# Performance work log

Measured on AMD Instinct MI355X. Metric: run time of the kernel, lower is better.

Reference implementation:

```python
import jax, jax.numpy as jnp
import numpy as np

B, N, K = 256, 1024, 64          # batch, atoms per structure, abc combinations
E = 2 * K                        # embedding_dim = 128
NSG = 230                        # number of space groups
LN_EPS = 1e-5


def setup_inputs() -> dict:
    key = jax.random.key(0)
    ks = jax.random.split(key, 12)
    xav = float(np.sqrt(6.0 / (K + K)))  # xavier_uniform bound for [K,K] slices
    return {
        "atom_positions": jax.random.uniform(ks[0], (B, N, 3), dtype=jnp.float32),
        "reciprocal_matrices": jax.random.normal(ks[1], (B, 3, 3), dtype=jnp.float32),
        "space_group": jax.random.randint(ks[2], (B, 1), 1, NSG + 1, dtype=jnp.int32),
        "abc_combinations": jax.random.normal(ks[3], (K, 3), dtype=jnp.float32),
        "graphs_array": jax.random.uniform(ks[4], (NSG, K, K), dtype=jnp.float32),
        "w_real": jax.random.uniform(ks[5], (NSG, K, K), jnp.float32, -xav, xav),
        "w_imag": jax.random.uniform(ks[6], (NSG, K, K), jnp.float32, -xav, xav),
        "b_real": jnp.zeros((NSG, K), jnp.float32),
        "b_imag": jnp.zeros((NSG, K), jnp.float32),
        "W2": jax.random.normal(ks[7], (E, E), dtype=jnp.float32) * 0.05,
        "b2": jnp.zeros((E,), jnp.float32),
        "gamma": jnp.ones((E,), jnp.float32),
        "beta": jnp.zeros((E,), jnp.float32),
    }


def reference(atom_positions, reciprocal_matrices, space_group, abc_combinations,
              graphs_array, w_real, w_imag, b_real, b_imag, W2, b2, gamma, beta):
    sg = space_group[:, 0] - 1                                  # [B] in [0,229]
    # transformed_abc = abc @ recip^T : [B,K,3]
    t_abc = jnp.einsum('kc,bdc->bkd', abc_combinations, reciprocal_matrices)
    # encodings = exp(i*2pi * pos @ t_abc^T) : [B,N,K] complex
    phase = (2.0 * jnp.pi) * jnp.einsum('bnc,bkc->bnk', atom_positions, t_abc)
    enc = jax.lax.complex(jnp.cos(phase), jnp.sin(phase))
    # per-sample adjacency gather + complex batched matmul
    adj = graphs_array[sg]                                      # [B,K,K]
    weighted = jnp.einsum('bnk,bkm->bnm', enc, adj.astype(enc.dtype))
    weighted = weighted[:, :, :K]                               # slice to embedding_dim//2
    # SpaceGroupDenseLayer: per-sample complex expert weights
    Wc = jax.lax.complex(w_real, w_imag)[sg]                    # [B,K,K]
    bc = jax.lax.complex(b_real, b_imag)[sg][:, None, :]        # [B,1,K]
    out_c = jnp.einsum('bni,bif->bnf', weighted, Wc) + bc       # [B,N,K] complex
    x = jnp.concatenate([out_c.real, out_c.imag], axis=-1)      # [B,N,2K]
    x = jax.nn.silu(x)
    x = x @ W2.T + b2                                           # Linear(E,E)
    mu = jnp.mean(x, axis=-1, keepdims=True)
    var = jnp.mean(jnp.square(x - mu), axis=-1, keepdims=True)
    return (x - mu) * jax.lax.rsqrt(var + LN_EPS) * gamma + beta
```

## Files before the change

kernel.cpp:

```cpp
#include <hip/hip_runtime.h>
#include <math.h>

#define BB 256
#define NN 1024
#define KK 64
#define EE 128
#define TM 64

typedef _Float16 half8 __attribute__((ext_vector_type(8)));
typedef __fp16 fp16x2 __attribute__((ext_vector_type(2)));
typedef float f32x4 __attribute__((ext_vector_type(4)));

__device__ __forceinline__ int swz(int row, int halfcol) {
    return (row * EE + halfcol) ^ ((row & 7) << 3);
}
__device__ __forceinline__ int swz64(int row, int halfcol) {
    return (row << 6) + (halfcol ^ ((row & 7) << 3));
}

__device__ __forceinline__ void gload_lds16(const void* g, void* l) {
    __builtin_amdgcn_global_load_lds(
        (const __attribute__((address_space(1))) unsigned int*)g,
        (__attribute__((address_space(3))) unsigned int*)l, 16, 0, 0);
}

__global__ __launch_bounds__(256) void prep_kernel(
    const float* __restrict__ recip,
    const int* __restrict__ space_group,
    const float* __restrict__ abc,
    const float* __restrict__ graphs,
    const float* __restrict__ w_real,
    const float* __restrict__ w_imag,
    const float* __restrict__ b_real,
    const float* __restrict__ b_imag,
    const float* __restrict__ W2,
    _Float16* __restrict__ Mt,
    float* __restrict__ bbout,
    float* __restrict__ tabcP,
    _Float16* __restrict__ W2h)
{
    const int b = blockIdx.x;
    const int t = threadIdx.x;
    const int sg = space_group[b] - 1;

    if (b < EE * EE / 256) {
        const int idx = b * 256 + t;
        W2h[idx] = (_Float16)W2[idx];
    }

    __shared__ float adjL[KK * KK];
    __shared__ float wrL[KK * KK];
    __shared__ float wiL[KK * KK];

    const float* adjG = graphs + (size_t)sg * KK * KK;
    const float* wrG  = w_real + (size_t)sg * KK * KK;
    const float* wiG  = w_imag + (size_t)sg * KK * KK;
    for (int idx = t; idx < KK * KK; idx += 256) {
        adjL[idx] = adjG[idx];
        wrL[idx]  = wrG[idx];
        wiL[idx]  = wiG[idx];
    }
    __syncthreads();

    const int i  = t >> 2;
    const int f0 = (t & 3) * 16;
    float cr[16], ci[16];
#pragma unroll
    for (int c = 0; c < 16; ++c) { cr[c] = 0.f; ci[c] = 0.f; }
    for (int k = 0; k < KK; ++k) {
        const float a = adjL[i * KK + k];
#pragma unroll
        for (int c = 0; c < 16; ++c) {
            cr[c] += a * wrL[k * KK + f0 + c];
            ci[c] += a * wiL[k * KK + f0 + c];
        }
    }
    _Float16* Mb = Mt + (size_t)b * EE * EE;
#pragma unroll
    for (int c = 0; c < 16; ++c) {
        const int f = f0 + c;
        Mb[f * EE + i]             = (_Float16)cr[c];
        Mb[f * EE + KK + i]        = (_Float16)(-ci[c]);
        Mb[(KK + f) * EE + i]      = (_Float16)ci[c];
        Mb[(KK + f) * EE + KK + i] = (_Float16)cr[c];
    }
    if (t < EE) {
        bbout[b * EE + t] = (t < KK) ? b_real[sg * KK + t] : b_imag[sg * KK + (t - KK)];
    }
    if (t < KK) {
        const float a0 = abc[t * 3 + 0], a1 = abc[t * 3 + 1], a2 = abc[t * 3 + 2];
        const float* R = recip + b * 9;
        float4 v;
        v.x = a0 * R[0] + a1 * R[1] + a2 * R[2];
        v.y = a0 * R[3] + a1 * R[4] + a2 * R[5];
        v.z = a0 * R[6] + a1 * R[7] + a2 * R[8];
        v.w = 0.f;
        *(float4*)&tabcP[((size_t)b * KK + t) * 4] = v;
    }
}

__global__ __launch_bounds__(256, 4) void main_kernel(
    const float* __restrict__ pos,
    const _Float16* __restrict__ Mt,
    const float* __restrict__ bball,
    const float* __restrict__ tabcP,
    const _Float16* __restrict__ W2h,
    const float* __restrict__ b2,
    const float* __restrict__ gamma,
    const float* __restrict__ beta,
    float* __restrict__ out)
{
    const int d = blockIdx.x;
    const int j  = d >> 3;
    const int b  = (d & 7) * 32 + (j >> 4);
    const int n0 = (j & 15) * TM;
    const int t  = threadIdx.x;
    const int w    = t >> 6;
    const int lane = t & 63;
    const int ln15 = lane & 15;
    const int kg   = lane >> 4;

    __shared__ __align__(16) _Float16 Bt[EE * EE];
    _Float16* X = Bt + (EE * EE) / 2;

    {
        const char* srcM = (const char*)(Mt + (size_t)b * EE * EE);
#pragma unroll
        for (int i = 0; i < 8; ++i) {
            const int c16 = t + i * 256;
            const int row = c16 >> 4;
            const int sl  = c16 & 15;
            const int g   = row * 16 + (sl ^ (row & 7));
            gload_lds16(srcM + g * 16, (char*)Bt + c16 * 16);
        }
    }

    const int grow = n0 + w * 16 + ln15;
    const float* pr = pos + ((size_t)b * NN + grow) * 3;
    const float px = pr[0], py = pr[1], pz = pr[2];
    const float* tp = tabcP + (size_t)b * KK * 4;

    half8 afrag[4];
#pragma unroll
    for (int mq = 0; mq < 2; ++mq) {
        _Float16 cb[8], sb[8];
#pragma unroll
        for (int jj = 0; jj < 8; ++jj) {
            const int k = mq * 32 + kg * 8 + jj;
            const float4 tv = *(const float4*)&tp[k * 4];
            const float rev = px * tv.x + py * tv.y + pz * tv.z;
            const float fr  = __builtin_amdgcn_fractf(rev);
            sb[jj] = (_Float16)__builtin_amdgcn_sinf(fr);
            cb[jj] = (_Float16)__builtin_amdgcn_cosf(fr);
        }
        afrag[mq]     = *(half8*)cb;
        afrag[mq + 2] = *(half8*)sb;
    }
    __syncthreads();

    __builtin_amdgcn_s_setprio(1);
    f32x4 acc[8];
#pragma unroll
    for (int nt = 0; nt < 8; ++nt) {
        const int n = nt * 16 + ln15;
        f32x4 a = {0.f, 0.f, 0.f, 0.f};
#pragma unroll
        for (int kc = 0; kc < 4; ++kc) {
            const half8 bf = *(const half8*)&Bt[swz(n, kc * 32 + kg * 8)];
            a = __builtin_amdgcn_mfma_f32_16x16x32_f16(bf, afrag[kc], a, 0, 0, 0);
        }
        acc[nt] = a;
    }
    __builtin_amdgcn_s_setprio(0);
    __syncthreads();

    {
        const char* srcW = (const char*)W2h;
#pragma unroll
        for (int i = 0; i < 4; ++i) {
            const int c = t + i * 256;
            const int n = c >> 3;
            const int s = c & 7;
            const int g = n * 16 + (s ^ (n & 7));
            gload_lds16(srcW + g * 16, (char*)Bt + c * 16);
        }
    }

    {
        const int xrow = w * 16 + ln15;
        const float* bbp = bball + b * EE;
#pragma unroll
        for (int nt = 0; nt < 8; ++nt) {
            const int cb0 = nt * 16 + kg * 4;
            const float4 bb4 = *(const float4*)&bbp[cb0];
            float sv[4];
            sv[0] = acc[nt][0] + bb4.x;
            sv[1] = acc[nt][1] + bb4.y;
            sv[2] = acc[nt][2] + bb4.z;
            sv[3] = acc[nt][3] + bb4.w;
#pragma unroll
            for (int r2 = 0; r2 < 4; ++r2)
                sv[r2] = sv[r2] * __builtin_amdgcn_rcpf(1.f + __expf(-sv[r2]));
            const fp16x2 p0 = __builtin_amdgcn_cvt_pkrtz(sv[0], sv[1]);
            const fp16x2 p1 = __builtin_amdgcn_cvt_pkrtz(sv[2], sv[3]);
            uint2 u;
            u.x = __builtin_bit_cast(unsigned int, p0);
            u.y = __builtin_bit_cast(unsigned int, p1);
            *(uint2*)&X[swz(xrow, cb0)] = u;
        }
    }

    const int arow = w * 16 + ln15;
    half8 a2[4];
#pragma unroll
    for (int kc = 0; kc < 4; ++kc)
        a2[kc] = *(const half8*)&X[swz(arow, kc * 32 + kg * 8)];
    __syncthreads();

    {
        const char* srcW = (const char*)W2h;
#pragma unroll
        for (int i = 0; i < 4; ++i) {
            const int c = t + i * 256;
            const int n = c >> 3;
            const int s = c & 7;
            const int g = n * 16 + 8 + (s ^ (n & 7));
            gload_lds16(srcW + g * 16, (char*)X + c * 16);
        }
    }

    __builtin_amdgcn_s_setprio(1);
    f32x4 acc2[8];
#pragma unroll
    for (int nt = 0; nt < 8; ++nt) {
        const int n = nt * 16 + ln15;
        f32x4 a = {0.f, 0.f, 0.f, 0.f};
#pragma unroll
        for (int kc = 0; kc < 2; ++kc) {
            const half8 bf = *(const half8*)&Bt[swz64(n, kc * 32 + kg * 8)];
            a = __builtin_amdgcn_mfma_f32_16x16x32_f16(a2[kc], bf, a, 0, 0, 0);
        }
        acc2[nt] = a;
    }
    __builtin_amdgcn_s_setprio(0);
    __syncthreads();

    __builtin_amdgcn_s_setprio(1);
#pragma unroll
    for (int nt = 0; nt < 8; ++nt) {
        const int n = nt * 16 + ln15;
        f32x4 a = acc2[nt];
#pragma unroll
        for (int kc = 0; kc < 2; ++kc) {
            const half8 bf = *(const half8*)&X[swz64(n, kc * 32 + kg * 8)];
            a = __builtin_amdgcn_mfma_f32_16x16x32_f16(a2[2 + kc], bf, a, 0, 0, 0);
        }
        acc2[nt] = a;
    }
    __builtin_amdgcn_s_setprio(0);

    float s[4] = {0.f, 0.f, 0.f, 0.f}, q[4] = {0.f, 0.f, 0.f, 0.f};
#pragma unroll
    for (int nt = 0; nt < 8; ++nt) {
        const int col = nt * 16 + ln15;
        const float b2v = b2[col];
#pragma unroll
        for (int r2 = 0; r2 < 4; ++r2) {
            const float v = acc2[nt][r2] + b2v;
            acc2[nt][r2] = v;
            s[r2] += v;
            q[r2] += v * v;
        }
    }
#pragma unroll
    for (int m = 1; m < 16; m <<= 1) {
#pragma unroll
        for (int r2 = 0; r2 < 4; ++r2) {
            s[r2] += __shfl_xor(s[r2], m);
            q[r2] += __shfl_xor(q[r2], m);
        }
    }
    const float inv = 1.f / EE;
    float mu[4], rs[4];
#pragma unroll
    for (int r2 = 0; r2 < 4; ++r2) {
        mu[r2] = s[r2] * inv;
        rs[r2] = __builtin_amdgcn_rsqf(fmaxf(q[r2] * inv - mu[r2] * mu[r2], 0.f) + 1e-5f);
    }
#pragma unroll
    for (int nt = 0; nt < 8; ++nt) {
        const int col = nt * 16 + ln15;
        const float g  = gamma[col];
        const float be = beta[col];
#pragma unroll
        for (int r2 = 0; r2 < 4; ++r2) {
            const int rr = w * 16 + kg * 4 + r2;
            out[((size_t)b * NN + n0 + rr) * EE + col] =
                (acc2[nt][r2] - mu[r2]) * rs[r2] * g + be;
        }
    }
}

extern "C" void kernel_launch(void* const* d_in, const int* in_sizes, int n_in,
                              void* d_out, int out_size, void* d_ws, size_t ws_size,
                              hipStream_t stream) {
    const float* pos    = (const float*)d_in[0];
    const float* recip  = (const float*)d_in[1];
    const int*   sgp    = (const int*)d_in[2];
    const float* abc    = (const float*)d_in[3];
    const float* graphs = (const float*)d_in[4];
    const float* wr     = (const float*)d_in[5];
    const float* wi     = (const float*)d_in[6];
    const float* br     = (const float*)d_in[7];
    const float* bi     = (const float*)d_in[8];
    const float* W2     = (const float*)d_in[9];
    const float* b2     = (const float*)d_in[10];
    const float* gm     = (const float*)d_in[11];
    const float* bt     = (const float*)d_in[12];
    float* out = (float*)d_out;

    char* ws = (char*)d_ws;
    _Float16* Mt    = (_Float16*)ws;
    char* p = ws + (size_t)BB * EE * EE * 2;
    _Float16* W2h   = (_Float16*)p;            p += EE * EE * 2;
    float*    bball = (float*)p;               p += (size_t)BB * EE * 4;
    float*    tabcP = (float*)p;

    hipLaunchKernelGGL(prep_kernel, dim3(BB), dim3(256), 0, stream,
                       recip, sgp, abc, graphs, wr, wi, br, bi, W2, Mt, bball, tabcP, W2h);
    hipLaunchKernelGGL(main_kernel, dim3(BB * NN / TM), dim3(256), 0, stream,
                       pos, Mt, bball, tabcP, W2h, b2, gm, bt, out);
}
```

Baseline: 62.98 us.

## Process two 64-row tiles per block to reuse staged matrices

Each block now handles 128 atom rows as two 64-row sub-tiles, so the per-sample fused matrix and the W2 halves loaded into shared memory are reused across twice the rows and the grid halves. The aim is to cut global-to-LDS staging traffic and per-block setup and barrier overhead. In exchange each thread holds twice the accumulators (acc0/acc1, acc2_0/acc2_1, a2_0/a2_1), which raises register pressure and may reduce occupancy under the launch bounds of 4 blocks per CU.

```diff
diff --git a/kernel.cpp b/kernel.cpp
--- a/kernel.cpp
+++ b/kernel.cpp
@@ -112,8 +112,8 @@
 {
     const int d = blockIdx.x;
     const int j  = d >> 3;
-    const int b  = (d & 7) * 32 + (j >> 4);
-    const int n0 = (j & 15) * TM;
+    const int b  = (d & 7) * 32 + (j >> 3);
+    const int n0 = (j & 7) * (2 * TM);
     const int t  = threadIdx.x;
     const int w    = t >> 6;
     const int lane = t & 63;
@@ -135,31 +135,32 @@
         }
     }
 
-    const int grow = n0 + w * 16 + ln15;
-    const float* pr = pos + ((size_t)b * NN + grow) * 3;
-    const float px = pr[0], py = pr[1], pz = pr[2];
     const float* tp = tabcP + (size_t)b * KK * 4;
+    const int rbase = n0 + w * 16 + ln15;
 
     half8 afrag[4];
-#pragma unroll
-    for (int mq = 0; mq < 2; ++mq) {
-        _Float16 cb[8], sb[8];
-#pragma unroll
-        for (int jj = 0; jj < 8; ++jj) {
-            const int k = mq * 32 + kg * 8 + jj;
-            const float4 tv = *(const float4*)&tp[k * 4];
-            const float rev = px * tv.x + py * tv.y + pz * tv.z;
-            const float fr  = __builtin_amdgcn_fractf(rev);
-            sb[jj] = (_Float16)__builtin_amdgcn_sinf(fr);
-            cb[jj] = (_Float16)__builtin_amdgcn_cosf(fr);
-        }
-        afrag[mq]     = *(half8*)cb;
-        afrag[mq + 2] = *(half8*)sb;
+    {
+        const float* pr = pos + ((size_t)b * NN + rbase) * 3;
+        const float px = pr[0], py = pr[1], pz = pr[2];
+#pragma unroll
+        for (int mq = 0; mq < 2; ++mq) {
+            _Float16 cb[8], sb[8];
+#pragma unroll
+            for (int jj = 0; jj < 8; ++jj) {
+                const int k = mq * 32 + kg * 8 + jj;
+                const float4 tv = *(const float4*)&tp[k * 4];
+                const float fr = __builtin_amdgcn_fractf(px * tv.x + py * tv.y + pz * tv.z);
+                sb[jj] = (_Float16)__builtin_amdgcn_sinf(fr);
+                cb[jj] = (_Float16)__builtin_amdgcn_cosf(fr);
+            }
+            afrag[mq]     = *(half8*)cb;
+            afrag[mq + 2] = *(half8*)sb;
+        }
     }
     __syncthreads();
 
     __builtin_amdgcn_s_setprio(1);
-    f32x4 acc[8];
+    f32x4 acc0[8];
 #pragma unroll
     for (int nt = 0; nt < 8; ++nt) {
         const int n = nt * 16 + ln15;
@@ -169,7 +170,41 @@
             const half8 bf = *(const half8*)&Bt[swz(n, kc * 32 + kg * 8)];
             a = __builtin_amdgcn_mfma_f32_16x16x32_f16(bf, afrag[kc], a, 0, 0, 0);
         }
-        acc[nt] = a;
+        acc0[nt] = a;
+    }
+    __builtin_amdgcn_s_setprio(0);
+
+    {
+        const float* pr = pos + ((size_t)b * NN + rbase + TM) * 3;
+        const float px = pr[0], py = pr[1], pz = pr[2];
+#pragma unroll
+        for (int mq = 0; mq < 2; ++mq) {
+            _Float16 cb[8], sb[8];
+#pragma unroll
+            for (int jj = 0; jj < 8; ++jj) {
+                const int k = mq * 32 + kg * 8 + jj;
+                const float4 tv = *(const float4*)&tp[k * 4];
+                const float fr = __builtin_amdgcn_fractf(px * tv.x + py * tv.y + pz * tv.z);
+                sb[jj] = (_Float16)__builtin_amdgcn_sinf(fr);
+                cb[jj] = (_Float16)__builtin_amdgcn_cosf(fr);
+            }
+            afrag[mq]     = *(half8*)cb;
+            afrag[mq + 2] = *(half8*)sb;
+        }
+    }
+
+    __builtin_amdgcn_s_setprio(1);
+    f32x4 acc1[8];
+#pragma unroll
+    for (int nt = 0; nt < 8; ++nt) {
+        const int n = nt * 16 + ln15;
+        f32x4 a = {0.f, 0.f, 0.f, 0.f};
+#pragma unroll
+        for (int kc = 0; kc < 4; ++kc) {
+            const half8 bf = *(const half8*)&Bt[swz(n, kc * 32 + kg * 8)];
+            a = __builtin_amdgcn_mfma_f32_16x16x32_f16(bf, afrag[kc], a, 0, 0, 0);
+        }
+        acc1[nt] = a;
     }
     __builtin_amdgcn_s_setprio(0);
     __syncthreads();
@@ -186,35 +221,53 @@
         }
     }
 
-    {
-        const int xrow = w * 16 + ln15;
-        const float* bbp = bball + b * EE;
-#pragma unroll
-        for (int nt = 0; nt < 8; ++nt) {
-            const int cb0 = nt * 16 + kg * 4;
-            const float4 bb4 = *(const float4*)&bbp[cb0];
-            float sv[4];
-            sv[0] = acc[nt][0] + bb4.x;
-            sv[1] = acc[nt][1] + bb4.y;
-            sv[2] = acc[nt][2] + bb4.z;
-            sv[3] = acc[nt][3] + bb4.w;
-#pragma unroll
-            for (int r2 = 0; r2 < 4; ++r2)
-                sv[r2] = sv[r2] * __builtin_amdgcn_rcpf(1.f + __expf(-sv[r2]));
-            const fp16x2 p0 = __builtin_amdgcn_cvt_pkrtz(sv[0], sv[1]);
-            const fp16x2 p1 = __builtin_amdgcn_cvt_pkrtz(sv[2], sv[3]);
-            uint2 u;
-            u.x = __builtin_bit_cast(unsigned int, p0);
-            u.y = __builtin_bit_cast(unsigned int, p1);
-            *(uint2*)&X[swz(xrow, cb0)] = u;
-        }
-    }
-
-    const int arow = w * 16 + ln15;
-    half8 a2[4];
+    const int xrow = w * 16 + ln15;
+    const float* bbp = bball + b * EE;
+    half8 a2_0[4], a2_1[4];
+#pragma unroll
+    for (int nt = 0; nt < 8; ++nt) {
+        const int cb0 = nt * 16 + kg * 4;
+        const float4 bb4 = *(const float4*)&bbp[cb0];
+        float sv[4];
+        sv[0] = acc0[nt][0] + bb4.x;
+        sv[1] = acc0[nt][1] + bb4.y;
+        sv[2] = acc0[nt][2] + bb4.z;
+        sv[3] = acc0[nt][3] + bb4.w;
+#pragma unroll
+        for (int r2 = 0; r2 < 4; ++r2)
+            sv[r2] = sv[r2] * __builtin_amdgcn_rcpf(1.f + __expf(-sv[r2]));
+        const fp16x2 p0 = __builtin_amdgcn_cvt_pkrtz(sv[0], sv[1]);
+        const fp16x2 p1 = __builtin_amdgcn_cvt_pkrtz(sv[2], sv[3]);
+        uint2 u;
+        u.x = __builtin_bit_cast(unsigned int, p0);
+        u.y = __builtin_bit_cast(unsigned int, p1);
+        *(uint2*)&X[swz(xrow, cb0)] = u;
+    }
 #pragma unroll
     for (int kc = 0; kc < 4; ++kc)
-        a2[kc] = *(const half8*)&X[swz(arow, kc * 32 + kg * 8)];
+        a2_0[kc] = *(const half8*)&X[swz(xrow, kc * 32 + kg * 8)];
+#pragma unroll
+    for (int nt = 0; nt < 8; ++nt) {
+        const int cb0 = nt * 16 + kg * 4;
+        const float4 bb4 = *(const float4*)&bbp[cb0];
+        float sv[4];
+        sv[0] = acc1[nt][0] + bb4.x;
+        sv[1] = acc1[nt][1] + bb4.y;
+        sv[2] = acc1[nt][2] + bb4.z;
+        sv[3] = acc1[nt][3] + bb4.w;
+#pragma unroll
+        for (int r2 = 0; r2 < 4; ++r2)
+            sv[r2] = sv[r2] * __builtin_amdgcn_rcpf(1.f + __expf(-sv[r2]));
+        const fp16x2 p0 = __builtin_amdgcn_cvt_pkrtz(sv[0], sv[1]);
+        const fp16x2 p1 = __builtin_amdgcn_cvt_pkrtz(sv[2], sv[3]);
+        uint2 u;
+        u.x = __builtin_bit_cast(unsigned int, p0);
+        u.y = __builtin_bit_cast(unsigned int, p1);
+        *(uint2*)&X[swz(xrow, cb0)] = u;
+    }
+#pragma unroll
+    for (int kc = 0; kc < 4; ++kc)
+        a2_1[kc] = *(const half8*)&X[swz(xrow, kc * 32 + kg * 8)];
     __syncthreads();
 
     {
@@ -230,17 +283,20 @@
     }
 
     __builtin_amdgcn_s_setprio(1);
-    f32x4 acc2[8];
+    f32x4 acc2_0[8], acc2_1[8];
 #pragma unroll
     for (int nt = 0; nt < 8; ++nt) {
         const int n = nt * 16 + ln15;
         f32x4 a = {0.f, 0.f, 0.f, 0.f};
+        f32x4 c = {0.f, 0.f, 0.f, 0.f};
 #pragma unroll
         for (int kc = 0; kc < 2; ++kc) {
             const half8 bf = *(const half8*)&Bt[swz64(n, kc * 32 + kg * 8)];
-            a = __builtin_amdgcn_mfma_f32_16x16x32_f16(a2[kc], bf, a, 0, 0, 0);
-        }
-        acc2[nt] = a;
+            a = __builtin_amdgcn_mfma_f32_16x16x32_f16(a2_0[kc], bf, a, 0, 0, 0);
+            c = __builtin_amdgcn_mfma_f32_16x16x32_f16(a2_1[kc], bf, c, 0, 0, 0);
+        }
+        acc2_0[nt] = a;
+        acc2_1[nt] = c;
     }
     __builtin_amdgcn_s_setprio(0);
     __syncthreads();
@@ -249,54 +305,61 @@
 #pragma unroll
     for (int nt = 0; nt < 8; ++nt) {
         const int n = nt * 16 + ln15;
-        f32x4 a = acc2[nt];
+        f32x4 a = acc2_0[nt];
+        f32x4 c = acc2_1[nt];
 #pragma unroll
         for (int kc = 0; kc < 2; ++kc) {
             const half8 bf = *(const half8*)&X[swz64(n, kc * 32 + kg * 8)];
-            a = __builtin_amdgcn_mfma_f32_16x16x32_f16(a2[2 + kc], bf, a, 0, 0, 0);
-        }
-        acc2[nt] = a;
+            a = __builtin_amdgcn_mfma_f32_16x16x32_f16(a2_0[2 + kc], bf, a, 0, 0, 0);
+            c = __builtin_amdgcn_mfma_f32_16x16x32_f16(a2_1[2 + kc], bf, c, 0, 0, 0);
+        }
+        acc2_0[nt] = a;
+        acc2_1[nt] = c;
     }
     __builtin_amdgcn_s_setprio(0);
 
-    float s[4] = {0.f, 0.f, 0.f, 0.f}, q[4] = {0.f, 0.f, 0.f, 0.f};
-#pragma unroll
-    for (int nt = 0; nt < 8; ++nt) {
-        const int col = nt * 16 + ln15;
-        const float b2v = b2[col];
+#pragma unroll
+    for (int tile = 0; tile < 2; ++tile) {
+        f32x4* A = (tile == 0) ? acc2_0 : acc2_1;
+        float s[4] = {0.f, 0.f, 0.f, 0.f}, q[4] = {0.f, 0.f, 0.f, 0.f};
+#pragma unroll
+        for (int nt = 0; nt < 8; ++nt) {
+            const int col = nt * 16 + ln15;
+            const float b2v = b2[col];
+#pragma unroll
+            for (int r2 = 0; r2 < 4; ++r2) {
+                const float v = A[nt][r2] + b2v;
+                A[nt][r2] = v;
+                s[r2] += v;
+                q[r2] += v * v;
+            }
+        }
+#pragma unroll
+        for (int m = 1; m < 16; m <<= 1) {
+#pragma unroll
+            for (int r2 = 0; r2 < 4; ++r2) {
+                s[r2] += __shfl_xor(s[r2], m);
+                q[r2] += __shfl_xor(q[r2], m);
+            }
+        }
+        const float inv = 1.f / EE;
+        float mu[4], rs[4];
 #pragma unroll
         for (int r2 = 0; r2 < 4; ++r2) {
-            const float v = acc2[nt][r2] + b2v;
-            acc2[nt][r2] = v;
-            s[r2] += v;
-            q[r2] += v * v;
-        }
-    }
-#pragma unroll
-    for (int m = 1; m < 16; m <<= 1) {
-#pragma unroll
-        for (int r2 = 0; r2 < 4; ++r2) {
-            s[r2] += __shfl_xor(s[r2], m);
-            q[r2] += __shfl_xor(q[r2], m);
-        }
-    }
-    const float inv = 1.f / EE;
-    float mu[4], rs[4];
-#pragma unroll
-    for (int r2 = 0; r2 < 4; ++r2) {
-        mu[r2] = s[r2] * inv;
-        rs[r2] = __builtin_amdgcn_rsqf(fmaxf(q[r2] * inv - mu[r2] * mu[r2], 0.f) + 1e-5f);
-    }
-#pragma unroll
-    for (int nt = 0; nt < 8; ++nt) {
-        const int col = nt * 16 + ln15;
-        const float g  = gamma[col];
-        const float be = beta[col];
-#pragma unroll
-        for (int r2 = 0; r2 < 4; ++r2) {
-            const int rr = w * 16 + kg * 4 + r2;
-            out[((size_t)b * NN + n0 + rr) * EE + col] =
-                (acc2[nt][r2] - mu[r2]) * rs[r2] * g + be;
+            mu[r2] = s[r2] * inv;
+            rs[r2] = __builtin_amdgcn_rsqf(fmaxf(q[r2] * inv - mu[r2] * mu[r2], 0.f) + 1e-5f);
+        }
+#pragma unroll
+        for (int nt = 0; nt < 8; ++nt) {
+            const int col = nt * 16 + ln15;
+            const float g  = gamma[col];
+            const float be = beta[col];
+#pragma unroll
+            for (int r2 = 0; r2 < 4; ++r2) {
+                const int rr = w * 16 + kg * 4 + r2;
+                out[((size_t)b * NN + n0 + tile * TM + rr) * EE + col] =
+                    (A[nt][r2] - mu[r2]) * rs[r2] * g + be;
+            }
         }
     }
 }
@@ -328,6 +391,6 @@
 
     hipLaunchKernelGGL(prep_kernel, dim3(BB), dim3(256), 0, stream,
                        recip, sgp, abc, graphs, wr, wi, br, bi, W2, Mt, bball, tabcP, W2h);
-    hipLaunchKernelGGL(main_kernel, dim3(BB * NN / TM), dim3(256), 0, stream,
+    hipLaunchKernelGGL(main_kernel, dim3(BB * NN / (2 * TM)), dim3(256), 0, stream,
                        pos, Mt, bball, tabcP, W2h, b2, gm, bt, out);
 }
```

Result: slower. 66.64 us (+5.8%).
